# Optimization experiments

Measured on AMD Instinct MI355X. Metric: run time of the kernel, lower is better.

The kernel has to match this reference:

```python
import jax, jax.numpy as jnp
import numpy as np
import math

B, S, D = 1, 2048, 512
H = 8
DH = D // H
WIN = 128  # window_size
EPS = 1e-5


def _layernorm(x, g, b):
    mu = jnp.mean(x, axis=-1, keepdims=True)
    var = jnp.mean((x - mu) ** 2, axis=-1, keepdims=True)
    return (x - mu) * jax.lax.rsqrt(var + EPS) * g + b


def _local_attention(q, k, v, window_size):
    # q,k,v: [B,H,S,DH]. Faithful to F.pad + unfold: zero-padded keys
    # participate in softmax with score 0 (no masking), as in the original.
    w = window_size // 2
    W = 2 * w + 1
    kp = jnp.pad(k, ((0, 0), (0, 0), (w, w), (0, 0)))
    vp = jnp.pad(v, ((0, 0), (0, 0), (w, w), (0, 0)))
    idx = jnp.arange(q.shape[2])[:, None] + jnp.arange(W)[None, :]  # [S,W]
    k_win = kp[:, :, idx]  # [B,H,S,W,DH]
    v_win = vp[:, :, idx]  # [B,H,S,W,DH]
    scores = jnp.einsum('bhsd,bhswd->bhsw', q, k_win) / math.sqrt(q.shape[-1])
    attn = jax.nn.softmax(scores, axis=-1)
    return jnp.einsum('bhsw,bhswd->bhsd', attn, v_win)


def setup_inputs() -> dict:
    key = jax.random.key(0)
    ks = jax.random.split(key, 8)
    sc = 0.02
    return {
        'x': jax.random.normal(ks[0], (B, S, D), dtype=jnp.float32),
        'w_qkv': jax.random.normal(ks[1], (D, 3 * D), dtype=jnp.float32) * sc,
        'b_qkv': jnp.zeros((3 * D,), dtype=jnp.float32),
        'w_out': jax.random.normal(ks[2], (D, D), dtype=jnp.float32) * sc,
        'b_out': jnp.zeros((D,), dtype=jnp.float32),
        'ln_g': jnp.ones((D,), dtype=jnp.float32),
        'ln_b': jnp.zeros((D,), dtype=jnp.float32),
        'w1': jax.random.normal(ks[3], (D, 4 * D), dtype=jnp.float32) * sc,
        'b1': jnp.zeros((4 * D,), dtype=jnp.float32),
        'w2': jax.random.normal(ks[4], (4 * D, D), dtype=jnp.float32) * sc,
        'b2': jnp.zeros((D,), dtype=jnp.float32),
    }


def reference(x, w_qkv, b_qkv, w_out, b_out, ln_g, ln_b, w1, b1, w2, b2):
    residual = x
    xn = _layernorm(x, ln_g, ln_b)
    qkv = xn @ w_qkv + b_qkv                       # [B,S,3D]
    qkv = qkv.reshape(B, S, 3, H, DH)
    qkv = jnp.transpose(qkv, (2, 0, 3, 1, 4))      # [3,B,H,S,DH]
    q, k, v = qkv[0], qkv[1], qkv[2]
    attn_out = _local_attention(q, k, v, WIN)       # [B,H,S,DH]
    attn_out = jnp.transpose(attn_out, (0, 2, 1, 3)).reshape(B, S, D)
    attn_out = attn_out @ w_out + b_out
    out = residual + attn_out
    # FFN applied directly to `out` (no second norm in original)
    ffn = jax.nn.gelu(out @ w1 + b1, approximate=False) @ w2 + b2
    return out + ffn
```

## Files before the change

### kernel.cpp

```cpp
#include <hip/hip_runtime.h>
#include <math.h>

#define S_LEN 2048
#define DMODEL 512
#define NHEAD 8
#define DHEAD 64
#define LN_EPS 1e-5f

typedef __bf16 bf16;
typedef __bf16 bf16x8 __attribute__((ext_vector_type(8)));
typedef __bf16 bf16x4 __attribute__((ext_vector_type(4)));
typedef __bf16 bf16x2 __attribute__((ext_vector_type(2)));
typedef float f32x4 __attribute__((ext_vector_type(4)));

__device__ __forceinline__ float wave_reduce_sum(float x) {
#pragma unroll
  for (int off = 32; off > 0; off >>= 1) x += __shfl_xor(x, off);
  return x;
}

__global__ __launch_bounds__(256) void prep_kernel(
    const float* __restrict__ x, const float* __restrict__ ln_g,
    const float* __restrict__ ln_b, const float* __restrict__ w_qkv,
    const float* __restrict__ w_out, const float* __restrict__ w1,
    const float* __restrict__ w2, bf16* __restrict__ xn,
    bf16* __restrict__ wqkvT, bf16* __restrict__ woutT,
    bf16* __restrict__ w1T, bf16* __restrict__ w2T) {
  __shared__ float t[32][33];
  int b = blockIdx.x;
  const int tid = threadIdx.x;
  if (b < 2048) {
    const float2 v = ((const float2*)(x + (size_t)b * DMODEL))[tid];
    float s = v.x + v.y;
    float s2 = v.x * v.x + v.y * v.y;
    s = wave_reduce_sum(s);
    s2 = wave_reduce_sum(s2);
    __shared__ float red[2][4];
    const int wv = tid >> 6, ln = tid & 63;
    if (ln == 0) { red[0][wv] = s; red[1][wv] = s2; }
    __syncthreads();
    s = red[0][0] + red[0][1] + red[0][2] + red[0][3];
    s2 = red[1][0] + red[1][1] + red[1][2] + red[1][3];
    const float mu = s * (1.0f / DMODEL);
    const float var = s2 * (1.0f / DMODEL) - mu * mu;
    const float rs = rsqrtf(var + LN_EPS);
    const float2 gg = ((const float2*)ln_g)[tid];
    const float2 bb = ((const float2*)ln_b)[tid];
    bf16x2 o;
    o[0] = (bf16)((v.x - mu) * rs * gg.x + bb.x);
    o[1] = (bf16)((v.y - mu) * rs * gg.y + bb.y);
    ((bf16x2*)(xn + (size_t)b * DMODEL))[tid] = o;
    return;
  }
  b -= 2048;
  const float* W; bf16* WT; int K, N, bx, by;
  if (b < 768)       { W = w_qkv; WT = wqkvT; K = 512;  N = 1536; bx = b % 48; by = b / 48; }
  else if (b < 1024) { b -= 768;  W = w_out; WT = woutT; K = 512;  N = 512;  bx = b % 16; by = b / 16; }
  else if (b < 2048) { b -= 1024; W = w1;    WT = w1T;   K = 512;  N = 2048; bx = b % 64; by = b / 64; }
  else               { b -= 2048; W = w2;    WT = w2T;   K = 2048; N = 512;  bx = b % 16; by = b / 16; }
  const int c = tid & 31, r8 = tid >> 5;
  const int n0 = bx * 32, k0 = by * 32;
#pragma unroll
  for (int it = 0; it < 4; it++) {
    const int r = r8 + it * 8;
    t[r][c] = W[(size_t)(k0 + r) * N + n0 + c];
  }
  __syncthreads();
#pragma unroll
  for (int it = 0; it < 4; it++) {
    const int r = r8 + it * 8;
    WT[(size_t)(n0 + r) * K + k0 + c] = (bf16)t[c][r];
  }
}

template <int MODE>
__device__ __forceinline__ void epilogue_store(float v, const float* res,
                                               float* Cf, bf16* Cb,
                                               size_t row, size_t col, int N) {
  if (MODE == 2) v = 0.5f * v * (1.0f + erff(v * 0.70710678118654752f));
  if (MODE == 1 || MODE == 3) v += res[row * N + col];
  if (MODE == 1 || MODE == 3) Cf[row * N + col] = v;
  if (MODE == 1 || MODE == 2) Cb[row * N + col] = (bf16)v;
}

template <int MODE>
__global__ __launch_bounds__(256) void mmC_kernel(const bf16* __restrict__ A,
                                                  const bf16* __restrict__ BT,
                                                  const float* __restrict__ bias,
                                                  bf16* __restrict__ Cb,
                                                  bf16* __restrict__ vT,
                                                  int N, int K) {
  __shared__ bf16 As[2][64 * 64];
  __shared__ bf16 Bs[2][64 * 64];
  const int tid = threadIdx.x;
  const int wave = tid >> 6, lane = tid & 63;
  const int lr = lane & 15, kg = lane >> 4;
  const int wm = wave & 1, wn = wave >> 1;
  const int rowBase = blockIdx.y * 64, colBase = blockIdx.x * 64;

  const bf16* aP[2]; const bf16* bP[2]; int aOff[2], bOff[2];
#pragma unroll
  for (int r = 0; r < 2; ++r) {
    const int c = wave * 2 + r;
    const int elem = c * 512 + lane * 8;
    const int s = elem >> 11, row = (elem >> 5) & 63, kp = elem & 31;
    aP[r] = A + (size_t)(rowBase + row) * K + s * 32 + kp;
    bP[r] = BT + (size_t)(colBase + row) * K + s * 32 + kp;
    aOff[r] = c * 512;
    bOff[r] = c * 512;
  }

  auto stage = [&](int kk, int buf) {
#pragma unroll
    for (int r = 0; r < 2; ++r) {
      __builtin_amdgcn_global_load_lds(
          (const __attribute__((address_space(1))) void*)(aP[r] + kk),
          (__attribute__((address_space(3))) void*)(&As[buf][aOff[r]]), 16, 0, 0);
      __builtin_amdgcn_global_load_lds(
          (const __attribute__((address_space(1))) void*)(bP[r] + kk),
          (__attribute__((address_space(3))) void*)(&Bs[buf][bOff[r]]), 16, 0, 0);
    }
  };

  f32x4 acc[2][2] = {};
  const int niter = K >> 6;

  stage(0, 0);
  for (int it = 0; it < niter; ++it) {
    const int cur = it & 1;
    __syncthreads();
    if (it + 1 < niter) stage((it + 1) << 6, cur ^ 1);
    const bf16* as = As[cur];
    const bf16* bs = Bs[cur];
#pragma unroll
    for (int s = 0; s < 2; ++s) {
      bf16x8 af[2], bfr[2];
#pragma unroll
      for (int i = 0; i < 2; ++i)
        af[i] = *(const bf16x8*)(as + s * 2048 + (wm * 32 + i * 16 + lr) * 32 + kg * 8);
#pragma unroll
      for (int j = 0; j < 2; ++j)
        bfr[j] = *(const bf16x8*)(bs + s * 2048 + (wn * 32 + j * 16 + lr) * 32 + kg * 8);
#pragma unroll
      for (int i = 0; i < 2; ++i)
#pragma unroll
        for (int j = 0; j < 2; ++j)
          acc[i][j] = __builtin_amdgcn_mfma_f32_16x16x32_bf16(af[i], bfr[j],
                                                              acc[i][j], 0, 0, 0);
    }
  }

#pragma unroll
  for (int j = 0; j < 2; ++j) {
    const int col = colBase + wn * 32 + j * 16 + lr;
    const float bs = bias[col];
    if (MODE == 4 && col >= 1024) {
      bf16* dst = vT + (size_t)(col - 1024) * S_LEN;
#pragma unroll
      for (int i = 0; i < 2; ++i) {
        bf16x4 p;
#pragma unroll
        for (int r = 0; r < 4; ++r) p[r] = (bf16)(acc[i][j][r] + bs);
        *(bf16x4*)(dst + rowBase + wm * 32 + i * 16 + kg * 4) = p;
      }
    } else {
#pragma unroll
      for (int i = 0; i < 2; ++i)
#pragma unroll
        for (int r = 0; r < 4; ++r) {
          const size_t row = rowBase + wm * 32 + i * 16 + kg * 4 + r;
          float v = acc[i][j][r] + bs;
          if (MODE == 2) v = 0.5f * v * (1.0f + erff(v * 0.70710678118654752f));
          Cb[row * N + col] = (bf16)v;
        }
    }
  }
}

template <int MODE>
__global__ __launch_bounds__(256) void mmB_kernel(const bf16* __restrict__ A,
                                                  const bf16* __restrict__ BT,
                                                  const float* __restrict__ bias,
                                                  const float* __restrict__ res,
                                                  float* __restrict__ Cf,
                                                  bf16* __restrict__ Cb,
                                                  int N, int K) {
  __shared__ bf16 As[2][32 * 64];
  __shared__ bf16 Bs[2][64 * 64];
  const int tid = threadIdx.x;
  const int wave = tid >> 6, lane = tid & 63;
  const int lr = lane & 15, kg = lane >> 4;
  const int rowBase = blockIdx.y * 32, colBase = blockIdx.x * 64;

  const bf16* aP; const bf16* bP[2]; int aOff, bOff[2];
  {
    const int elem = wave * 512 + lane * 8;
    const int s = elem >> 10, row = (elem >> 5) & 31, kp = elem & 31;
    aP = A + (size_t)(rowBase + row) * K + s * 32 + kp;
    aOff = wave * 512;
  }
#pragma unroll
  for (int r = 0; r < 2; ++r) {
    const int c = wave * 2 + r;
    const int elem = c * 512 + lane * 8;
    const int s = elem >> 11, row = (elem >> 5) & 63, kp = elem & 31;
    bP[r] = BT + (size_t)(colBase + row) * K + s * 32 + kp;
    bOff[r] = c * 512;
  }

  auto stage = [&](int kk, int buf) {
    __builtin_amdgcn_global_load_lds(
        (const __attribute__((address_space(1))) void*)(aP + kk),
        (__attribute__((address_space(3))) void*)(&As[buf][aOff]), 16, 0, 0);
#pragma unroll
    for (int r = 0; r < 2; ++r)
      __builtin_amdgcn_global_load_lds(
          (const __attribute__((address_space(1))) void*)(bP[r] + kk),
          (__attribute__((address_space(3))) void*)(&Bs[buf][bOff[r]]), 16, 0, 0);
  };

  f32x4 acc[2] = {};
  const int niter = K >> 6;

  stage(0, 0);
  for (int it = 0; it < niter; ++it) {
    const int cur = it & 1;
    __syncthreads();
    if (it + 1 < niter) stage((it + 1) << 6, cur ^ 1);
    const bf16* as = As[cur];
    const bf16* bs = Bs[cur];
#pragma unroll
    for (int s = 0; s < 2; ++s) {
      bf16x8 af[2], bfr;
#pragma unroll
      for (int i = 0; i < 2; ++i)
        af[i] = *(const bf16x8*)(as + s * 1024 + (i * 16 + lr) * 32 + kg * 8);
      bfr = *(const bf16x8*)(bs + s * 2048 + (wave * 16 + lr) * 32 + kg * 8);
#pragma unroll
      for (int i = 0; i < 2; ++i)
        acc[i] = __builtin_amdgcn_mfma_f32_16x16x32_bf16(af[i], bfr, acc[i], 0, 0, 0);
    }
  }

  {
    const int col = colBase + wave * 16 + lr;
    const float bs = bias[col];
#pragma unroll
    for (int i = 0; i < 2; ++i)
#pragma unroll
      for (int r = 0; r < 4; ++r)
        epilogue_store<MODE>(acc[i][r] + bs, res, Cf, Cb,
                             (size_t)(rowBase + i * 16 + kg * 4 + r),
                             (size_t)col, N);
  }
}

__global__ __launch_bounds__(256) void attn_fused(const bf16* __restrict__ qkvb,
                                                  const bf16* __restrict__ vT,
                                                  bf16* __restrict__ attnb) {
  __shared__ bf16 Kl[192][72];
  __shared__ bf16 Vt[64][200];
  __shared__ bf16 Ql[64][72];

  const int tid = threadIdx.x;
  const int s0 = blockIdx.x * 64;
  const int hc = blockIdx.y * DHEAD;

  {
    const int row = tid >> 2, c0 = (tid & 3) * 16;
    const bf16* src = qkvb + (size_t)(s0 + row) * 1536 + hc + c0;
    *(bf16x8*)&Ql[row][c0] = *(const bf16x8*)src;
    *(bf16x8*)&Ql[row][c0 + 8] = *(const bf16x8*)(src + 8);
  }
#pragma unroll
  for (int it = 0; it < 3; it++) {
    const int row = it * 64 + (tid >> 2), c0 = (tid & 3) * 16;
    const int p = s0 - 64 + row;
    bf16x8 a, b;
    if (p >= 0 && p < S_LEN) {
      const bf16* src = qkvb + (size_t)p * 1536 + 512 + hc + c0;
      a = *(const bf16x8*)src;
      b = *(const bf16x8*)(src + 8);
    } else {
#pragma unroll
      for (int j = 0; j < 8; j++) { a[j] = (bf16)0.f; b[j] = (bf16)0.f; }
    }
    *(bf16x8*)&Kl[row][c0] = a;
    *(bf16x8*)&Kl[row][c0 + 8] = b;
  }
  {
    const int d = tid >> 2, r0 = (tid & 3) * 48;
    const bf16* src = vT + (size_t)(hc + d) * S_LEN;
#pragma unroll
    for (int i = 0; i < 6; i++) {
      const int p0 = s0 - 64 + r0 + i * 8;
      bf16x8 v;
      if (p0 >= 0 && p0 + 8 <= S_LEN) {
        v = *(const bf16x8*)(src + p0);
      } else {
#pragma unroll
        for (int j = 0; j < 8; j++) {
          const int p = p0 + j;
          v[j] = (p >= 0 && p < S_LEN) ? src[p] : (bf16)0.f;
        }
      }
      *(bf16x8*)&Vt[d][r0 + i * 8] = v;
    }
  }
  __syncthreads();

  const int wv = tid >> 6, lane = tid & 63;
  const int lr = lane & 15, kg = lane >> 4;

  f32x4 c[12] = {};
#pragma unroll
  for (int step = 0; step < 2; step++) {
    const bf16x8 qf = *(const bf16x8*)&Ql[wv * 16 + lr][step * 32 + kg * 8];
#pragma unroll
    for (int t = 0; t < 12; t++) {
      const bf16x8 kf = *(const bf16x8*)&Kl[t * 16 + lr][step * 32 + kg * 8];
      c[t] = __builtin_amdgcn_mfma_f32_16x16x32_bf16(qf, kf, c[t], 0, 0, 0);
    }
  }

  float e[12][4];
  float inv[4];
#pragma unroll
  for (int rr = 0; rr < 4; rr++) {
    const int q = wv * 16 + kg * 4 + rr;
    float m = -1e30f;
#pragma unroll
    for (int t = 0; t < 12; t++) {
      const int col = t * 16 + lr;
      if (col >= q && col <= q + 128) m = fmaxf(m, c[t][rr] * 0.125f);
    }
#pragma unroll
    for (int off = 1; off < 16; off <<= 1) m = fmaxf(m, __shfl_xor(m, off));
    float sum = 0.f;
#pragma unroll
    for (int t = 0; t < 12; t++) {
      const int col = t * 16 + lr;
      const bool valid = (col >= q) && (col <= q + 128);
      const float ev = valid ? __expf(c[t][rr] * 0.125f - m) : 0.f;
      e[t][rr] = ev;
      sum += ev;
    }
#pragma unroll
    for (int off = 1; off < 16; off <<= 1) sum += __shfl_xor(sum, off);
    inv[rr] = 1.f / sum;
  }

  __syncthreads();

  bf16* Pl = (bf16*)Kl + wv * (16 * 200);
#pragma unroll
  for (int rr = 0; rr < 4; rr++)
#pragma unroll
    for (int t = 0; t < 12; t++)
      Pl[(kg * 4 + rr) * 200 + t * 16 + lr] = (bf16)(e[t][rr] * inv[rr]);

  f32x4 o[4] = {};
#pragma unroll
  for (int step = 0; step < 6; step++) {
    const bf16x8 pf = *(const bf16x8*)&Pl[lr * 200 + step * 32 + kg * 8];
#pragma unroll
    for (int jt = 0; jt < 4; jt++) {
      const bf16x8 vf = *(const bf16x8*)&Vt[jt * 16 + lr][step * 32 + kg * 8];
      o[jt] = __builtin_amdgcn_mfma_f32_16x16x32_bf16(pf, vf, o[jt], 0, 0, 0);
    }
  }

#pragma unroll
  for (int jt = 0; jt < 4; jt++)
#pragma unroll
    for (int rr = 0; rr < 4; rr++) {
      const int q = wv * 16 + kg * 4 + rr;
      attnb[(size_t)(s0 + q) * DMODEL + hc + jt * 16 + lr] = (bf16)o[jt][rr];
    }
}

extern "C" void kernel_launch(void* const* d_in, const int* in_sizes, int n_in,
                              void* d_out, int out_size, void* d_ws, size_t ws_size,
                              hipStream_t stream) {
  const float* x     = (const float*)d_in[0];
  const float* w_qkv = (const float*)d_in[1];
  const float* b_qkv = (const float*)d_in[2];
  const float* w_out = (const float*)d_in[3];
  const float* b_out = (const float*)d_in[4];
  const float* ln_g  = (const float*)d_in[5];
  const float* ln_b  = (const float*)d_in[6];
  const float* w1    = (const float*)d_in[7];
  const float* b1    = (const float*)d_in[8];
  const float* w2    = (const float*)d_in[9];
  const float* b2    = (const float*)d_in[10];
  float* out = (float*)d_out;

  char* w = (char*)d_ws;
  const size_t MB = 1u << 20;
  bf16* xn    = (bf16*)(w + 0);
  bf16* attnb = (bf16*)(w + 0);
  bf16* qkvb  = (bf16*)(w + 2 * MB);
  bf16* outb  = (bf16*)(w + 2 * MB);
  bf16* vT    = (bf16*)(w + 8 * MB);
  bf16* h1    = (bf16*)(w + 10 * MB);
  bf16* wqkvT = (bf16*)(w + 18 * MB);
  bf16* woutT = (bf16*)(w + 19 * MB + 512 * 1024);
  bf16* w1T   = (bf16*)(w + 20 * MB);
  bf16* w2T   = (bf16*)(w + 22 * MB);

  prep_kernel<<<5120, 256, 0, stream>>>(x, ln_g, ln_b, w_qkv, w_out, w1, w2,
                                        xn, wqkvT, woutT, w1T, w2T);
  mmC_kernel<4><<<dim3(24, 32), 256, 0, stream>>>(xn, wqkvT, b_qkv, qkvb, vT,
                                                  1536, 512);
  attn_fused<<<dim3(32, 8), 256, 0, stream>>>(qkvb, vT, attnb);
  mmB_kernel<1><<<dim3(8, 64), 256, 0, stream>>>(attnb, woutT, b_out, x, out,
                                                 outb, 512, 512);
  mmC_kernel<2><<<dim3(32, 32), 256, 0, stream>>>(outb, w1T, b1, h1, nullptr,
                                                  2048, 512);
  mmB_kernel<3><<<dim3(8, 64), 256, 0, stream>>>(h1, w2T, b2, out, out,
                                                 nullptr, 512, 2048);
}
```

Baseline: 141.6 us.

## Replace LDS-staged GEMMs with direct-load 128-tile MFMA kernels and split-K FFN2

Replaces the LDS double-buffered GEMM kernels with a register-direct MFMA core where each wave computes a 64x64 or 64x32 tile, read straight from global memory without shared-memory staging. The weight transposes for w_out, w1 and w2 now run inside the QKV GEMM launch as extra blocks, overlapping with it. FFN2 is split across K into two halves that accumulate into the output with atomic adds. The aim is fewer barriers and launches and more reuse per wave, at the cost of uncoalesced-ish global fragment loads, fewer blocks (low occupancy with launch_bounds 1), and nondeterministic atomic accumulation.

Result: slower. 179.4 us (+26.7%).

```diff
diff --git a/kernel.cpp b/kernel.cpp
--- a/kernel.cpp
+++ b/kernel.cpp
@@ -19,14 +19,31 @@
   return x;
 }
 
-__global__ __launch_bounds__(256) void prep_kernel(
+__device__ __forceinline__ void transpose_tile(const float* __restrict__ W,
+                                               bf16* __restrict__ WT, int K,
+                                               int N, int bx, int by,
+                                               float (*t)[33], int tid) {
+  const int c = tid & 31, r8 = tid >> 5;
+  const int n0 = bx * 32, k0 = by * 32;
+#pragma unroll
+  for (int it = 0; it < 4; it++) {
+    const int r = r8 + it * 8;
+    t[r][c] = W[(size_t)(k0 + r) * N + n0 + c];
+  }
+  __syncthreads();
+#pragma unroll
+  for (int it = 0; it < 4; it++) {
+    const int r = r8 + it * 8;
+    WT[(size_t)(n0 + r) * K + k0 + c] = (bf16)t[c][r];
+  }
+}
+
+__global__ __launch_bounds__(256) void prep1_kernel(
     const float* __restrict__ x, const float* __restrict__ ln_g,
     const float* __restrict__ ln_b, const float* __restrict__ w_qkv,
-    const float* __restrict__ w_out, const float* __restrict__ w1,
-    const float* __restrict__ w2, bf16* __restrict__ xn,
-    bf16* __restrict__ wqkvT, bf16* __restrict__ woutT,
-    bf16* __restrict__ w1T, bf16* __restrict__ w2T) {
+    bf16* __restrict__ xn, bf16* __restrict__ wqkvT) {
   __shared__ float t[32][33];
+  __shared__ float red[2][4];
   int b = blockIdx.x;
   const int tid = threadIdx.x;
   if (b < 2048) {
@@ -35,7 +52,6 @@
     float s2 = v.x * v.x + v.y * v.y;
     s = wave_reduce_sum(s);
     s2 = wave_reduce_sum(s2);
-    __shared__ float red[2][4];
     const int wv = tid >> 6, ln = tid & 63;
     if (ln == 0) { red[0][wv] = s; red[1][wv] = s2; }
     __syncthreads();
@@ -53,205 +69,177 @@
     return;
   }
   b -= 2048;
-  const float* W; bf16* WT; int K, N, bx, by;
-  if (b < 768)       { W = w_qkv; WT = wqkvT; K = 512;  N = 1536; bx = b % 48; by = b / 48; }
-  else if (b < 1024) { b -= 768;  W = w_out; WT = woutT; K = 512;  N = 512;  bx = b % 16; by = b / 16; }
-  else if (b < 2048) { b -= 1024; W = w1;    WT = w1T;   K = 512;  N = 2048; bx = b % 64; by = b / 64; }
-  else               { b -= 2048; W = w2;    WT = w2T;   K = 2048; N = 512;  bx = b % 16; by = b / 16; }
-  const int c = tid & 31, r8 = tid >> 5;
-  const int n0 = bx * 32, k0 = by * 32;
-#pragma unroll
-  for (int it = 0; it < 4; it++) {
-    const int r = r8 + it * 8;
-    t[r][c] = W[(size_t)(k0 + r) * N + n0 + c];
-  }
-  __syncthreads();
-#pragma unroll
-  for (int it = 0; it < 4; it++) {
-    const int r = r8 + it * 8;
-    WT[(size_t)(n0 + r) * K + k0 + c] = (bf16)t[c][r];
-  }
-}
-
-template <int MODE>
-__device__ __forceinline__ void epilogue_store(float v, const float* res,
-                                               float* Cf, bf16* Cb,
-                                               size_t row, size_t col, int N) {
-  if (MODE == 2) v = 0.5f * v * (1.0f + erff(v * 0.70710678118654752f));
-  if (MODE == 1 || MODE == 3) v += res[row * N + col];
-  if (MODE == 1 || MODE == 3) Cf[row * N + col] = v;
-  if (MODE == 1 || MODE == 2) Cb[row * N + col] = (bf16)v;
-}
-
-template <int MODE>
-__global__ __launch_bounds__(256) void mmC_kernel(const bf16* __restrict__ A,
-                                                  const bf16* __restrict__ BT,
-                                                  const float* __restrict__ bias,
-                                                  bf16* __restrict__ Cb,
-                                                  bf16* __restrict__ vT,
-                                                  int N, int K) {
-  __shared__ bf16 As[2][64 * 64];
-  __shared__ bf16 Bs[2][64 * 64];
-  const int tid = threadIdx.x;
+  transpose_tile(w_qkv, wqkvT, 512, 1536, b % 48, b / 48, t, tid);
+}
+
+template <int KLOOP, int JT>
+__device__ __forceinline__ void gemm_core(const bf16* __restrict__ A,
+                                          const bf16* __restrict__ BT,
+                                          int ldk, int waveRow, int waveCol,
+                                          int lr, int kg, f32x4 (&acc)[4][JT]) {
+  const bf16* ap = A + (size_t)(waveRow + lr) * ldk + kg * 8;
+  const bf16* bp = BT + (size_t)(waveCol + lr) * ldk + kg * 8;
+  const size_t rstride = (size_t)16 * ldk;
+#pragma unroll
+  for (int kk = 0; kk < KLOOP; kk += 32) {
+    bf16x8 af[4], bfv[JT];
+#pragma unroll
+    for (int i = 0; i < 4; i++)
+      af[i] = *(const bf16x8*)(ap + kk + i * rstride);
+#pragma unroll
+    for (int j = 0; j < JT; j++)
+      bfv[j] = *(const bf16x8*)(bp + kk + j * rstride);
+#pragma unroll
+    for (int i = 0; i < 4; i++)
+#pragma unroll
+      for (int j = 0; j < JT; j++)
+        acc[i][j] = __builtin_amdgcn_mfma_f32_16x16x32_bf16(af[i], bfv[j],
+                                                            acc[i][j], 0, 0, 0);
+  }
+}
+
+__global__ __launch_bounds__(256, 1) void qkv_kernel(
+    const bf16* __restrict__ A, const bf16* __restrict__ BT,
+    const float* __restrict__ bias, bf16* __restrict__ qkvb,
+    bf16* __restrict__ vT, const float* __restrict__ w_out,
+    const float* __restrict__ w1, const float* __restrict__ w2,
+    bf16* __restrict__ woutT, bf16* __restrict__ w1T, bf16* __restrict__ w2T) {
+  __shared__ float t[32][33];
+  int b = blockIdx.x;
+  const int tid = threadIdx.x;
+
+  if (b >= 192) {
+    b -= 192;
+    if (b < 256)       transpose_tile(w_out, woutT, 512, 512, b % 16, b / 16, t, tid);
+    else if (b < 1280) { b -= 256;  transpose_tile(w1, w1T, 512, 2048, b % 64, b / 64, t, tid); }
+    else               { b -= 1280; transpose_tile(w2, w2T, 2048, 512, b % 16, b / 16, t, tid); }
+    return;
+  }
+
   const int wave = tid >> 6, lane = tid & 63;
   const int lr = lane & 15, kg = lane >> 4;
   const int wm = wave & 1, wn = wave >> 1;
-  const int rowBase = blockIdx.y * 64, colBase = blockIdx.x * 64;
-
-  const bf16* aP[2]; const bf16* bP[2]; int aOff[2], bOff[2];
-#pragma unroll
-  for (int r = 0; r < 2; ++r) {
-    const int c = wave * 2 + r;
-    const int elem = c * 512 + lane * 8;
-    const int s = elem >> 11, row = (elem >> 5) & 63, kp = elem & 31;
-    aP[r] = A + (size_t)(rowBase + row) * K + s * 32 + kp;
-    bP[r] = BT + (size_t)(colBase + row) * K + s * 32 + kp;
-    aOff[r] = c * 512;
-    bOff[r] = c * 512;
-  }
-
-  auto stage = [&](int kk, int buf) {
-#pragma unroll
-    for (int r = 0; r < 2; ++r) {
-      __builtin_amdgcn_global_load_lds(
-          (const __attribute__((address_space(1))) void*)(aP[r] + kk),
-          (__attribute__((address_space(3))) void*)(&As[buf][aOff[r]]), 16, 0, 0);
-      __builtin_amdgcn_global_load_lds(
-          (const __attribute__((address_space(1))) void*)(bP[r] + kk),
-          (__attribute__((address_space(3))) void*)(&Bs[buf][bOff[r]]), 16, 0, 0);
-    }
-  };
-
-  f32x4 acc[2][2] = {};
-  const int niter = K >> 6;
-
-  stage(0, 0);
-  for (int it = 0; it < niter; ++it) {
-    const int cur = it & 1;
-    __syncthreads();
-    if (it + 1 < niter) stage((it + 1) << 6, cur ^ 1);
-    const bf16* as = As[cur];
-    const bf16* bs = Bs[cur];
-#pragma unroll
-    for (int s = 0; s < 2; ++s) {
-      bf16x8 af[2], bfr[2];
-#pragma unroll
-      for (int i = 0; i < 2; ++i)
-        af[i] = *(const bf16x8*)(as + s * 2048 + (wm * 32 + i * 16 + lr) * 32 + kg * 8);
-#pragma unroll
-      for (int j = 0; j < 2; ++j)
-        bfr[j] = *(const bf16x8*)(bs + s * 2048 + (wn * 32 + j * 16 + lr) * 32 + kg * 8);
-#pragma unroll
-      for (int i = 0; i < 2; ++i)
-#pragma unroll
-        for (int j = 0; j < 2; ++j)
-          acc[i][j] = __builtin_amdgcn_mfma_f32_16x16x32_bf16(af[i], bfr[j],
-                                                              acc[i][j], 0, 0, 0);
-    }
-  }
-
-#pragma unroll
-  for (int j = 0; j < 2; ++j) {
-    const int col = colBase + wn * 32 + j * 16 + lr;
+  const int waveRow = (b / 12) * 128 + wm * 64;
+  const int waveCol = (b % 12) * 128 + wn * 64;
+
+  f32x4 acc[4][4] = {};
+  gemm_core<512, 4>(A, BT, 512, waveRow, waveCol, lr, kg, acc);
+
+#pragma unroll
+  for (int j = 0; j < 4; j++) {
+    const int colT = waveCol + j * 16;
+    const int col = colT + lr;
     const float bs = bias[col];
-    if (MODE == 4 && col >= 1024) {
+    if (colT >= 1024) {
       bf16* dst = vT + (size_t)(col - 1024) * S_LEN;
 #pragma unroll
-      for (int i = 0; i < 2; ++i) {
+      for (int i = 0; i < 4; i++) {
         bf16x4 p;
 #pragma unroll
-        for (int r = 0; r < 4; ++r) p[r] = (bf16)(acc[i][j][r] + bs);
-        *(bf16x4*)(dst + rowBase + wm * 32 + i * 16 + kg * 4) = p;
+        for (int r = 0; r < 4; r++) p[r] = (bf16)(acc[i][j][r] + bs);
+        *(bf16x4*)(dst + waveRow + i * 16 + kg * 4) = p;
       }
     } else {
 #pragma unroll
-      for (int i = 0; i < 2; ++i)
-#pragma unroll
-        for (int r = 0; r < 4; ++r) {
-          const size_t row = rowBase + wm * 32 + i * 16 + kg * 4 + r;
-          float v = acc[i][j][r] + bs;
-          if (MODE == 2) v = 0.5f * v * (1.0f + erff(v * 0.70710678118654752f));
-          Cb[row * N + col] = (bf16)v;
+      for (int i = 0; i < 4; i++)
+#pragma unroll
+        for (int r = 0; r < 4; r++) {
+          const size_t row = waveRow + i * 16 + kg * 4 + r;
+          qkvb[row * 1536 + col] = (bf16)(acc[i][j][r] + bs);
         }
     }
   }
 }
 
-template <int MODE>
-__global__ __launch_bounds__(256) void mmB_kernel(const bf16* __restrict__ A,
-                                                  const bf16* __restrict__ BT,
-                                                  const float* __restrict__ bias,
-                                                  const float* __restrict__ res,
-                                                  float* __restrict__ Cf,
-                                                  bf16* __restrict__ Cb,
-                                                  int N, int K) {
-  __shared__ bf16 As[2][32 * 64];
-  __shared__ bf16 Bs[2][64 * 64];
+__global__ __launch_bounds__(256, 1) void outproj_kernel(
+    const bf16* __restrict__ A, const bf16* __restrict__ BT,
+    const float* __restrict__ bias, const float* __restrict__ res,
+    float* __restrict__ Cf, bf16* __restrict__ Cb) {
+  const int b = blockIdx.x;
   const int tid = threadIdx.x;
   const int wave = tid >> 6, lane = tid & 63;
   const int lr = lane & 15, kg = lane >> 4;
-  const int rowBase = blockIdx.y * 32, colBase = blockIdx.x * 64;
-
-  const bf16* aP; const bf16* bP[2]; int aOff, bOff[2];
-  {
-    const int elem = wave * 512 + lane * 8;
-    const int s = elem >> 10, row = (elem >> 5) & 31, kp = elem & 31;
-    aP = A + (size_t)(rowBase + row) * K + s * 32 + kp;
-    aOff = wave * 512;
-  }
-#pragma unroll
-  for (int r = 0; r < 2; ++r) {
-    const int c = wave * 2 + r;
-    const int elem = c * 512 + lane * 8;
-    const int s = elem >> 11, row = (elem >> 5) & 63, kp = elem & 31;
-    bP[r] = BT + (size_t)(colBase + row) * K + s * 32 + kp;
-    bOff[r] = c * 512;
-  }
-
-  auto stage = [&](int kk, int buf) {
-    __builtin_amdgcn_global_load_lds(
-        (const __attribute__((address_space(1))) void*)(aP + kk),
-        (__attribute__((address_space(3))) void*)(&As[buf][aOff]), 16, 0, 0);
-#pragma unroll
-    for (int r = 0; r < 2; ++r)
-      __builtin_amdgcn_global_load_lds(
-          (const __attribute__((address_space(1))) void*)(bP[r] + kk),
-          (__attribute__((address_space(3))) void*)(&Bs[buf][bOff[r]]), 16, 0, 0);
-  };
-
-  f32x4 acc[2] = {};
-  const int niter = K >> 6;
-
-  stage(0, 0);
-  for (int it = 0; it < niter; ++it) {
-    const int cur = it & 1;
-    __syncthreads();
-    if (it + 1 < niter) stage((it + 1) << 6, cur ^ 1);
-    const bf16* as = As[cur];
-    const bf16* bs = Bs[cur];
-#pragma unroll
-    for (int s = 0; s < 2; ++s) {
-      bf16x8 af[2], bfr;
-#pragma unroll
-      for (int i = 0; i < 2; ++i)
-        af[i] = *(const bf16x8*)(as + s * 1024 + (i * 16 + lr) * 32 + kg * 8);
-      bfr = *(const bf16x8*)(bs + s * 2048 + (wave * 16 + lr) * 32 + kg * 8);
-#pragma unroll
-      for (int i = 0; i < 2; ++i)
-        acc[i] = __builtin_amdgcn_mfma_f32_16x16x32_bf16(af[i], bfr, acc[i], 0, 0, 0);
-    }
-  }
-
-  {
-    const int col = colBase + wave * 16 + lr;
+  const int wm = wave & 1, wn = wave >> 1;
+  const int waveRow = (b / 8) * 128 + wm * 64;
+  const int waveCol = (b % 8) * 64 + wn * 32;
+
+  f32x4 acc[4][2] = {};
+  gemm_core<512, 2>(A, BT, 512, waveRow, waveCol, lr, kg, acc);
+
+#pragma unroll
+  for (int j = 0; j < 2; j++) {
+    const int col = waveCol + j * 16 + lr;
     const float bs = bias[col];
 #pragma unroll
-    for (int i = 0; i < 2; ++i)
-#pragma unroll
-      for (int r = 0; r < 4; ++r)
-        epilogue_store<MODE>(acc[i][r] + bs, res, Cf, Cb,
-                             (size_t)(rowBase + i * 16 + kg * 4 + r),
-                             (size_t)col, N);
+    for (int i = 0; i < 4; i++)
+#pragma unroll
+      for (int r = 0; r < 4; r++) {
+        const size_t row = waveRow + i * 16 + kg * 4 + r;
+        const float v = acc[i][j][r] + bs + res[row * DMODEL + col];
+        Cf[row * DMODEL + col] = v;
+        Cb[row * DMODEL + col] = (bf16)v;
+      }
+  }
+}
+
+__global__ __launch_bounds__(256, 1) void ffn1_kernel(
+    const bf16* __restrict__ A, const bf16* __restrict__ BT,
+    const float* __restrict__ bias, bf16* __restrict__ Cb) {
+  const int b = blockIdx.x;
+  const int tid = threadIdx.x;
+  const int wave = tid >> 6, lane = tid & 63;
+  const int lr = lane & 15, kg = lane >> 4;
+  const int wm = wave & 1, wn = wave >> 1;
+  const int waveRow = (b / 16) * 128 + wm * 64;
+  const int waveCol = (b % 16) * 128 + wn * 64;
+
+  f32x4 acc[4][4] = {};
+  gemm_core<512, 4>(A, BT, 512, waveRow, waveCol, lr, kg, acc);
+
+#pragma unroll
+  for (int j = 0; j < 4; j++) {
+    const int col = waveCol + j * 16 + lr;
+    const float bs = bias[col];
+#pragma unroll
+    for (int i = 0; i < 4; i++)
+#pragma unroll
+      for (int r = 0; r < 4; r++) {
+        const size_t row = waveRow + i * 16 + kg * 4 + r;
+        float v = acc[i][j][r] + bs;
+        v = 0.5f * v * (1.0f + erff(v * 0.70710678118654752f));
+        Cb[row * 2048 + col] = (bf16)v;
+      }
+  }
+}
+
+__global__ __launch_bounds__(256, 1) void ffn2_kernel(
+    const bf16* __restrict__ A, const bf16* __restrict__ BT,
+    const float* __restrict__ bias, float* __restrict__ out) {
+  const int b = blockIdx.x;
+  const int kh = b & 1;
+  const int tile = b >> 1;
+  const int tid = threadIdx.x;
+  const int wave = tid >> 6, lane = tid & 63;
+  const int lr = lane & 15, kg = lane >> 4;
+  const int wm = wave & 1, wn = wave >> 1;
+  const int waveRow = (tile / 8) * 128 + wm * 64;
+  const int waveCol = (tile % 8) * 64 + wn * 32;
+
+  f32x4 acc[4][2] = {};
+  gemm_core<1024, 2>(A + kh * 1024, BT + kh * 1024, 2048, waveRow, waveCol,
+                     lr, kg, acc);
+
+#pragma unroll
+  for (int j = 0; j < 2; j++) {
+    const int col = waveCol + j * 16 + lr;
+    const float bs = (kh == 0) ? bias[col] : 0.0f;
+#pragma unroll
+    for (int i = 0; i < 4; i++)
+#pragma unroll
+      for (int r = 0; r < 4; r++) {
+        const size_t row = waveRow + i * 16 + kg * 4 + r;
+        unsafeAtomicAdd(&out[row * DMODEL + col], acc[i][j][r] + bs);
+      }
   }
 }
 
@@ -408,15 +396,11 @@
   bf16* w1T   = (bf16*)(w + 20 * MB);
   bf16* w2T   = (bf16*)(w + 22 * MB);
 
-  prep_kernel<<<5120, 256, 0, stream>>>(x, ln_g, ln_b, w_qkv, w_out, w1, w2,
-                                        xn, wqkvT, woutT, w1T, w2T);
-  mmC_kernel<4><<<dim3(24, 32), 256, 0, stream>>>(xn, wqkvT, b_qkv, qkvb, vT,
-                                                  1536, 512);
+  prep1_kernel<<<2816, 256, 0, stream>>>(x, ln_g, ln_b, w_qkv, xn, wqkvT);
+  qkv_kernel<<<2496, 256, 0, stream>>>(xn, wqkvT, b_qkv, qkvb, vT,
+                                       w_out, w1, w2, woutT, w1T, w2T);
   attn_fused<<<dim3(32, 8), 256, 0, stream>>>(qkvb, vT, attnb);
-  mmB_kernel<1><<<dim3(8, 64), 256, 0, stream>>>(attnb, woutT, b_out, x, out,
-                                                 outb, 512, 512);
-  mmC_kernel<2><<<dim3(32, 32), 256, 0, stream>>>(outb, w1T, b1, h1, nullptr,
-                                                  2048, 512);
-  mmB_kernel<3><<<dim3(8, 64), 256, 0, stream>>>(h1, w2T, b2, out, out,
-                                                 nullptr, 512, 2048);
-}
+  outproj_kernel<<<128, 256, 0, stream>>>(attnb, woutT, b_out, x, out, outb);
+  ffn1_kernel<<<256, 256, 0, stream>>>(outb, w1T, b1, h1);
+  ffn2_kernel<<<256, 256, 0, stream>>>(h1, w2T, b2, out);
+}
```
